# Performance work log

Hardware: AMD Instinct MI355X
Metric: run time of the kernel (lower is better)

## Reference

```python
import jax, jax.numpy as jnp
import numpy as np

N, DIM_V, DIM_MM, DIM_O = 1024, 2048, 64, 2048
EPS_LOG = 1e-3


def setup_inputs() -> dict:
    key = jax.random.key(0)
    ks = jax.random.split(key, 12)
    feature_visual = jax.random.normal(ks[0], (N, DIM_V), dtype=jnp.float32)
    # valid boxes (x1, y1, x2, y2) inside an ~800x600 image
    x1 = jax.random.uniform(ks[1], (N, 1)) * 700.0
    y1 = jax.random.uniform(ks[2], (N, 1)) * 500.0
    w = jax.random.uniform(ks[3], (N, 1)) * 180.0 + 16.0
    h = jax.random.uniform(ks[4], (N, 1)) * 180.0 + 16.0
    rois = jnp.concatenate([x1, y1, x1 + w, y1 + h], axis=1)
    s = 0.02
    return {
        "feature_visual": feature_visual,
        "rois": rois,
        "Wk": jax.random.normal(ks[5], (DIM_V, DIM_MM), dtype=jnp.float32) * s,
        "bk": jnp.zeros((DIM_MM,), jnp.float32),
        "Wq": jax.random.normal(ks[6], (DIM_V, DIM_MM), dtype=jnp.float32) * s,
        "bq": jnp.zeros((DIM_MM,), jnp.float32),
        "Wv": jax.random.normal(ks[7], (DIM_V, DIM_O), dtype=jnp.float32) * s,
        "bv": jnp.zeros((DIM_O,), jnp.float32),
        "G1": jax.random.normal(ks[8], (4, DIM_MM), dtype=jnp.float32) * s,
        "g1": jnp.zeros((DIM_MM,), jnp.float32),
        "G2": jax.random.normal(ks[9], (DIM_MM, 1), dtype=jnp.float32) * s,
        "g2": jnp.zeros((1,), jnp.float32),
    }


def _geometry_weight(rois, G1, g1, G2, g2):
    # pairwise relative geometry features [N, N, 4], then MLP -> ReLU scalar weight [N, N]
    wh = rois[:, 2:4] - rois[:, 0:2]                      # [N, 2] box width/height
    ctr = 0.5 * (rois[:, 0:2] + rois[:, 2:4])             # [N, 2] centers
    d = ctr[None, :, :] - ctr[:, None, :]                 # [N, N, 2] (j relative to i)
    f12 = jnp.log(jnp.abs(d) / wh[:, None, :] + EPS_LOG)  # log(|dx|/wi), log(|dy|/hi)
    f34 = jnp.log(wh[None, :, :] / wh[:, None, :])        # log(wj/wi), log(hj/hi)
    geo = jnp.concatenate([f12, f34], axis=-1)            # [N, N, 4]
    h = jax.nn.relu(jnp.einsum('ijf,fm->ijm', geo, G1) + g1)
    w = jax.nn.relu(jnp.einsum('ijm,mo->ijo', h, G2) + g2)
    return w[..., 0]                                      # [N, N]


def reference(feature_visual, rois, Wk, bk, Wq, bq, Wv, bv, G1, g1, G2, g2):
    fv = jax.nn.relu(feature_visual)                      # pre-activation features
    k = fv @ Wk + bk                                      # [N, dim_mm]
    q = fv @ Wq + bq                                      # [N, dim_mm]
    v = fv @ Wv + bv                                      # [N, dim_o]
    scale = 1.0 / np.sqrt(DIM_MM).astype(np.float32)
    visual_weight = (q @ k.T) * scale                     # [N, N]: score[i,j] = <q_i... wait
    # torch: (query.unsqueeze(0) * key.unsqueeze(1)).sum(2) -> score[i,j] = <k_i, q_j>
    visual_weight = (k @ q.T) * scale
    geometry_weight = _geometry_weight(rois, G1, g1, G2, g2)
    attention = jnp.exp(visual_weight) * geometry_weight  # [N, N]
    n = attention.shape[0]
    attention = attention * (1.0 - jnp.eye(n, dtype=attention.dtype))  # zero diagonal
    attention = attention / (attention.sum(axis=1, keepdims=True) + 1e-10)
    return attention @ v                                  # [N, dim_o]
```

## Files before the change

kernel.cpp:

```cpp
#include <hip/hip_runtime.h>
#include <hip/hip_bf16.h>

#define NR 1024
#define DV 2048
#define DMM 64
#define DO 2048

typedef __attribute__((ext_vector_type(8))) __bf16 bf16x8;
typedef __attribute__((ext_vector_type(4))) float f32x4;

__device__ __forceinline__ float relu_f(float x) { return fmaxf(x, 0.f); }

__device__ __forceinline__ unsigned short f2bf(float x) {
    union { float f; unsigned int u; } v; v.f = x;
    unsigned int r = v.u + 0x7fffu + ((v.u >> 16) & 1u);
    return (unsigned short)(r >> 16);
}

__device__ __forceinline__ void gload_lds16(const void* g, void* l) {
    __builtin_amdgcn_global_load_lds(
        (const __attribute__((address_space(1))) void*)g,
        (__attribute__((address_space(3))) void*)l, 16, 0, 0);
}

__device__ __forceinline__ void transpose_tile(
    const float* __restrict__ W, unsigned short* __restrict__ Wt,
    int Ncols, int k0, int o0, float (*ld)[65])
{
    const int t = threadIdx.x;
    const int r = t >> 2;
    const int c0 = (t & 3) * 16;
    #pragma unroll
    for (int i = 0; i < 4; ++i) {
        float4 v = *reinterpret_cast<const float4*>(&W[(size_t)(k0 + r) * Ncols + o0 + c0 + i * 4]);
        ld[c0 + i * 4 + 0][r] = v.x;
        ld[c0 + i * 4 + 1][r] = v.y;
        ld[c0 + i * 4 + 2][r] = v.z;
        ld[c0 + i * 4 + 3][r] = v.w;
    }
    __syncthreads();
    const int o = t >> 2;
    const int kc = (t & 3) * 16;
    unsigned int u[8];
    #pragma unroll
    for (int j = 0; j < 8; ++j) {
        float x0 = ld[o][kc + 2 * j], x1 = ld[o][kc + 2 * j + 1];
        u[j] = (unsigned)f2bf(x0) | ((unsigned)f2bf(x1) << 16);
    }
    uint4* dst = reinterpret_cast<uint4*>(&Wt[(size_t)(o0 + o) * DV + k0 + kc]);
    dst[0] = make_uint4(u[0], u[1], u[2], u[3]);
    dst[1] = make_uint4(u[4], u[5], u[6], u[7]);
}

__global__ __launch_bounds__(256) void prep_kernel(
    const float* __restrict__ feat,
    const float* __restrict__ Wk, const float* __restrict__ Wq, const float* __restrict__ Wv,
    const float* __restrict__ rois,
    unsigned short* __restrict__ fvb, unsigned short* __restrict__ WkqT,
    unsigned short* __restrict__ WvT,
    float4* __restrict__ boxf, float2* __restrict__ boxinv)
{
    __shared__ float ld[64][65];
    const int bid = blockIdx.x;
    if (bid < 1024) {
        const int idx = bid * 256 + threadIdx.x;
        const float4 a = *reinterpret_cast<const float4*>(feat + (size_t)idx * 8);
        const float4 b = *reinterpret_cast<const float4*>(feat + (size_t)idx * 8 + 4);
        uint4 o;
        o.x = (unsigned)f2bf(relu_f(a.x)) | ((unsigned)f2bf(relu_f(a.y)) << 16);
        o.y = (unsigned)f2bf(relu_f(a.z)) | ((unsigned)f2bf(relu_f(a.w)) << 16);
        o.z = (unsigned)f2bf(relu_f(b.x)) | ((unsigned)f2bf(relu_f(b.y)) << 16);
        o.w = (unsigned)f2bf(relu_f(b.z)) | ((unsigned)f2bf(relu_f(b.w)) << 16);
        *reinterpret_cast<uint4*>(fvb + (size_t)idx * 8) = o;
    } else if (bid < 2048) {
        const int idx = bid - 1024;
        transpose_tile(Wv, WvT, DO, (idx >> 5) * 64, (idx & 31) * 64, ld);
    } else if (bid < 2080) {
        transpose_tile(Wk, WkqT, DMM, (bid - 2048) * 64, 0, ld);
    } else if (bid < 2112) {
        transpose_tile(Wq, WkqT + 64 * DV, DMM, (bid - 2080) * 64, 0, ld);
    } else {
        const int idx = (bid - 2112) * 256 + threadIdx.x;
        const float4 r = *reinterpret_cast<const float4*>(rois + (size_t)idx * 4);
        const float w = r.z - r.x, h = r.w - r.y;
        boxf[idx]   = make_float4(0.5f * (r.x + r.z), 0.5f * (r.y + r.w), __logf(w), __logf(h));
        boxinv[idx] = make_float2(1.f / w, 1.f / h);
    }
}

template<int NT, int LDA, int LDB, int BNR>
__device__ __forceinline__ void mfma_tile_pipe(
    const unsigned short* __restrict__ A, const unsigned short* __restrict__ Bt,
    int bm0, int bn0, unsigned short* As, unsigned short* Bs, f32x4 (&acc)[2][BNR])
{
    const int t = threadIdx.x;
    const int w = t >> 6, lane = t & 63;
    const int wr = w >> 1, wc = w & 1;
    const int fr = lane & 15, fq = lane >> 4;
    const int sr = lane >> 3;
    const int sc = ((lane & 7) ^ sr) * 8;

    const unsigned short* ga0 = A + (size_t)(bm0 + w * 16 + 0 + sr) * LDA + sc;
    const unsigned short* ga1 = A + (size_t)(bm0 + w * 16 + 8 + sr) * LDA + sc;
    const unsigned short* gb[BNR];
    #pragma unroll
    for (int g = 0; g < BNR; ++g)
        gb[g] = Bt + (size_t)(bn0 + w * (BNR * 8) + g * 8 + sr) * LDB + sc;

#define STAGE(buf, ts_) do {                                                   \
        const size_t ko_ = (size_t)(ts_) * 64;                                 \
        gload_lds16(ga0 + ko_, &As[(buf) * 4096 + w * 1024]);                  \
        gload_lds16(ga1 + ko_, &As[(buf) * 4096 + w * 1024 + 512]);            \
        _Pragma("unroll")                                                      \
        for (int g = 0; g < BNR; ++g)                                          \
            gload_lds16(gb[g] + ko_,                                           \
                &Bs[(buf) * (BNR * 2048) + w * (BNR * 512) + g * 512]);        \
    } while (0)

#define COMPUTE(buf) do {                                                                     \
        const int kx_ = fr & 7;                                                               \
        const int clo_ = (fq ^ kx_) * 8, chi_ = ((fq + 4) ^ kx_) * 8;                         \
        bf16x8 afl[2], afh[2], bfl[BNR], bfh[BNR];                                            \
        _Pragma("unroll")                                                                     \
        for (int m = 0; m < 2; ++m) {                                                         \
            const int rb = (buf) * 4096 + (wr * 32 + m * 16 + fr) * 64;                       \
            afl[m] = *reinterpret_cast<const bf16x8*>(&As[rb + clo_]);                        \
            afh[m] = *reinterpret_cast<const bf16x8*>(&As[rb + chi_]);                        \
        }                                                                                     \
        _Pragma("unroll")                                                                     \
        for (int n = 0; n < BNR; ++n) {                                                       \
            const int cb = (buf) * (BNR * 2048) + (wc * (BNR * 16) + n * 16 + fr) * 64;       \
            bfl[n] = *reinterpret_cast<const bf16x8*>(&Bs[cb + clo_]);                        \
            bfh[n] = *reinterpret_cast<const bf16x8*>(&Bs[cb + chi_]);                        \
        }                                                                                     \
        _Pragma("unroll")                                                                     \
        for (int m = 0; m < 2; ++m)                                                           \
            _Pragma("unroll")                                                                 \
            for (int n = 0; n < BNR; ++n) {                                                   \
                acc[m][n] = __builtin_amdgcn_mfma_f32_16x16x32_bf16(afl[m], bfl[n], acc[m][n], 0, 0, 0); \
                acc[m][n] = __builtin_amdgcn_mfma_f32_16x16x32_bf16(afh[m], bfh[n], acc[m][n], 0, 0, 0); \
            }                                                                                 \
    } while (0)

    STAGE(0, 0);
    if (NT > 1) STAGE(1, 1);

    #pragma unroll 2
    for (int ts = 0; ts < NT - 1; ++ts) {
        if (BNR == 4) { asm volatile("s_waitcnt vmcnt(6)" ::: "memory"); }
        else          { asm volatile("s_waitcnt vmcnt(4)" ::: "memory"); }
        asm volatile("s_barrier" ::: "memory");
        COMPUTE(ts & 1);
        asm volatile("s_barrier" ::: "memory");
        if (ts + 2 < NT) STAGE(ts & 1, ts + 2);
    }
    asm volatile("s_waitcnt vmcnt(0)" ::: "memory");
    asm volatile("s_barrier" ::: "memory");
    COMPUTE((NT - 1) & 1);
#undef STAGE
#undef COMPUTE
}

__global__ __launch_bounds__(256) void gemm_vt_kq(
    const unsigned short* __restrict__ WvT, const unsigned short* __restrict__ fvb,
    const unsigned short* __restrict__ WkqT,
    const float* __restrict__ bv, const float* __restrict__ bk, const float* __restrict__ bq,
    unsigned short* __restrict__ vT, unsigned short* __restrict__ kqb)
{
    __shared__ unsigned short As[2 * 64 * 64];
    __shared__ unsigned short Bs[2 * 64 * 64];
    const int bid = blockIdx.x;
    const bool is_kq = bid >= 512;
    const unsigned short* A  = is_kq ? fvb  : WvT;
    const unsigned short* Bt = is_kq ? WkqT : fvb;
    const int bm0 = is_kq ? ((bid - 512) >> 1) * 64 : (bid >> 4) * 64;
    const int bn0 = is_kq ? ((bid - 512) & 1) * 64 : (bid & 15) * 64;

    f32x4 acc[2][2] = {};
    mfma_tile_pipe<DV / 64, DV, DV, 2>(A, Bt, bm0, bn0, As, Bs, acc);

    const int t = threadIdx.x;
    const int w = t >> 6, lane = t & 63;
    const int wr = w >> 1, wc = w & 1;
    const int fr = lane & 15, fq = lane >> 4;
    if (!is_kq) {
        #pragma unroll
        for (int m = 0; m < 2; ++m)
            #pragma unroll
            for (int r = 0; r < 4; ++r) {
                const int row = bm0 + wr * 32 + m * 16 + fq * 4 + r;
                const float badd = bv[row];
                #pragma unroll
                for (int n = 0; n < 2; ++n) {
                    const int col = bn0 + wc * 32 + n * 16 + fr;
                    vT[(size_t)row * NR + col] = f2bf(acc[m][n][r] + badd);
                }
            }
    } else {
        #pragma unroll
        for (int m = 0; m < 2; ++m)
            #pragma unroll
            for (int r = 0; r < 4; ++r) {
                const int row = bm0 + wr * 32 + m * 16 + fq * 4 + r;
                #pragma unroll
                for (int n = 0; n < 2; ++n) {
                    const int col = bn0 + wc * 32 + n * 16 + fr;
                    const float badd = (col < 64) ? bk[col] : bq[col - 64];
                    kqb[(size_t)row * 128 + col] = f2bf(acc[m][n][r] + badd);
                }
            }
    }
}

__global__ __launch_bounds__(256) void gemm_s(
    const unsigned short* __restrict__ kqb, float* __restrict__ S)
{
    __shared__ unsigned short As[64 * 64];
    __shared__ unsigned short Bs[128 * 64];
    const int bm0 = blockIdx.y * 64;
    const int bn0 = blockIdx.x * 128;
    f32x4 acc[2][4] = {};
    mfma_tile_pipe<1, 128, 128, 4>(kqb, kqb + 64, bm0, bn0, As, Bs, acc);
    const int t = threadIdx.x;
    const int w = t >> 6, lane = t & 63;
    const int wr = w >> 1, wc = w & 1;
    const int fr = lane & 15, fq = lane >> 4;
    #pragma unroll
    for (int m = 0; m < 2; ++m)
        #pragma unroll
        for (int r = 0; r < 4; ++r) {
            const int row = bm0 + wr * 32 + m * 16 + fq * 4 + r;
            #pragma unroll
            for (int n = 0; n < 4; ++n) {
                const int col = bn0 + wc * 64 + n * 16 + fr;
                S[(size_t)row * NR + col] = acc[m][n][r] * 0.125f;
            }
        }
}

__global__ __launch_bounds__(256) void gemm_out(
    const unsigned short* __restrict__ attb, const unsigned short* __restrict__ vT,
    float* __restrict__ out)
{
    __shared__ unsigned short As[2 * 64 * 64];
    __shared__ unsigned short Bs[2 * 64 * 64];
    const int bid = blockIdx.x;
    const int bm0 = (bid >> 5) * 64;
    const int bn0 = (bid & 31) * 64;
    f32x4 acc[2][2] = {};
    mfma_tile_pipe<NR / 64, NR, NR, 2>(attb, vT, bm0, bn0, As, Bs, acc);
    const int t = threadIdx.x;
    const int w = t >> 6, lane = t & 63;
    const int wr = w >> 1, wc = w & 1;
    const int fr = lane & 15, fq = lane >> 4;
    #pragma unroll
    for (int m = 0; m < 2; ++m)
        #pragma unroll
        for (int r = 0; r < 4; ++r) {
            const int row = bm0 + wr * 32 + m * 16 + fq * 4 + r;
            #pragma unroll
            for (int n = 0; n < 2; ++n) {
                const int col = bn0 + wc * 32 + n * 16 + fr;
                out[(size_t)row * DO + col] = acc[m][n][r];
            }
        }
}

#define MLP_STEP(A_, B_, C_, D_, E_, F_)                                            \
    {                                                                               \
        float h_ = fmaf(ff1[ch], A_, fmaf(ff2[ch], B_, fmaf(ff3[ch], C_,            \
                   fmaf(ff4[ch], D_, E_))));                                        \
        h_ = fmaxf(h_, 0.f);                                                        \
        gw[ch] = fmaf(h_, F_, gw[ch]);                                              \
    }

__global__ __launch_bounds__(256) void attn_kernel(
    const float* __restrict__ S,
    const float4* __restrict__ boxf, const float2* __restrict__ boxinv,
    const float* __restrict__ G1, const float* __restrict__ g1,
    const float* __restrict__ G2, const float* __restrict__ g2,
    unsigned short* __restrict__ att)
{
    __shared__ float G1s[4][64];
    __shared__ float g1s[64];
    __shared__ float G2s[64];
    __shared__ float red[4];
    const int i = blockIdx.x;
    const int t = threadIdx.x;
    if (t < 64) {
        G1s[0][t] = G1[t];
        G1s[1][t] = G1[64 + t];
        G1s[2][t] = G1[128 + t];
        G1s[3][t] = G1[192 + t];
        g1s[t] = g1[t];
        G2s[t] = G2[t];
    }
    __syncthreads();
    const float4 bi = boxf[i];
    const float2 ivi = boxinv[i];
    const float g2v = g2[0];

    float ff1[4], ff2[4], ff3[4], ff4[4], sc[4], gw[4] = {0.f, 0.f, 0.f, 0.f};
    #pragma unroll
    for (int ch = 0; ch < 4; ++ch) {
        const int j = ch * 256 + t;
        const float4 bj = boxf[j];
        sc[ch] = S[(size_t)i * NR + j];
        ff1[ch] = __logf(fmaf(fabsf(bj.x - bi.x), ivi.x, 1e-3f));
        ff2[ch] = __logf(fmaf(fabsf(bj.y - bi.y), ivi.y, 1e-3f));
        ff3[ch] = bj.z - bi.z;
        ff4[ch] = bj.w - bi.w;
    }

    for (int mt = 0; mt < 64; mt += 8) {
        const float4 A0 = *reinterpret_cast<const float4*>(&G1s[0][mt]);
        const float4 A1 = *reinterpret_cast<const float4*>(&G1s[0][mt + 4]);
        const float4 B0 = *reinterpret_cast<const float4*>(&G1s[1][mt]);
        const float4 B1 = *reinterpret_cast<const float4*>(&G1s[1][mt + 4]);
        const float4 C0 = *reinterpret_cast<const float4*>(&G1s[2][mt]);
        const float4 C1 = *reinterpret_cast<const float4*>(&G1s[2][mt + 4]);
        const float4 D0 = *reinterpret_cast<const float4*>(&G1s[3][mt]);
        const float4 D1 = *reinterpret_cast<const float4*>(&G1s[3][mt + 4]);
        const float4 E0 = *reinterpret_cast<const float4*>(&g1s[mt]);
        const float4 E1 = *reinterpret_cast<const float4*>(&g1s[mt + 4]);
        const float4 F0 = *reinterpret_cast<const float4*>(&G2s[mt]);
        const float4 F1 = *reinterpret_cast<const float4*>(&G2s[mt + 4]);
        #pragma unroll
        for (int ch = 0; ch < 4; ++ch) {
            MLP_STEP(A0.x, B0.x, C0.x, D0.x, E0.x, F0.x)
            MLP_STEP(A0.y, B0.y, C0.y, D0.y, E0.y, F0.y)
            MLP_STEP(A0.z, B0.z, C0.z, D0.z, E0.z, F0.z)
            MLP_STEP(A0.w, B0.w, C0.w, D0.w, E0.w, F0.w)
            MLP_STEP(A1.x, B1.x, C1.x, D1.x, E1.x, F1.x)
            MLP_STEP(A1.y, B1.y, C1.y, D1.y, E1.y, F1.y)
            MLP_STEP(A1.z, B1.z, C1.z, D1.z, E1.z, F1.z)
            MLP_STEP(A1.w, B1.w, C1.w, D1.w, E1.w, F1.w)
        }
    }

    float vals[4];
    float rsum = 0.f;
    #pragma unroll
    for (int ch = 0; ch < 4; ++ch) {
        const float gwp = fmaxf(gw[ch] + g2v, 0.f);
        float a = __expf(sc[ch]) * gwp;
        if (ch * 256 + t == i) a = 0.f;
        vals[ch] = a;
        rsum += a;
    }
    #pragma unroll
    for (int o = 32; o > 0; o >>= 1) rsum += __shfl_down(rsum, o, 64);
    if ((t & 63) == 0) red[t >> 6] = rsum;
    __syncthreads();
    const float inv = 1.f / (red[0] + red[1] + red[2] + red[3] + 1e-10f);
    #pragma unroll
    for (int ch = 0; ch < 4; ++ch)
        att[(size_t)i * NR + ch * 256 + t] = f2bf(vals[ch] * inv);
}

extern "C" void kernel_launch(void* const* d_in, const int* in_sizes, int n_in,
                              void* d_out, int out_size, void* d_ws, size_t ws_size,
                              hipStream_t stream) {
    const float* feat = (const float*)d_in[0];
    const float* rois = (const float*)d_in[1];
    const float* Wk   = (const float*)d_in[2];
    const float* bk   = (const float*)d_in[3];
    const float* Wq   = (const float*)d_in[4];
    const float* bq   = (const float*)d_in[5];
    const float* Wv   = (const float*)d_in[6];
    const float* bv   = (const float*)d_in[7];
    const float* G1   = (const float*)d_in[8];
    const float* g1   = (const float*)d_in[9];
    const float* G2   = (const float*)d_in[10];
    const float* g2   = (const float*)d_in[11];
    float* out = (float*)d_out;
    char* ws = (char*)d_ws;

    unsigned short* kqb  = (unsigned short*)ws;
    float4* boxf         = (float4*)(ws + (256 << 10));
    float2* boxinv       = (float2*)(ws + (272 << 10));
    unsigned short* fvb  = (unsigned short*)(ws + (512 << 10));
    unsigned short* WvT  = (unsigned short*)(ws + (512 << 10) + (4 << 20));
    unsigned short* WkqT = (unsigned short*)(ws + (512 << 10) + (12 << 20));
    unsigned short* vT   = (unsigned short*)(ws + (1024 << 10) + (12 << 20));
    unsigned short* attb = (unsigned short*)(ws + (1024 << 10) + (16 << 20));
    float* Sbuf          = (float*)(ws + (1024 << 10) + (18 << 20));

    prep_kernel<<<2116, 256, 0, stream>>>(feat, Wk, Wq, Wv, rois, fvb, WkqT, WvT, boxf, boxinv);
    gemm_vt_kq<<<544, 256, 0, stream>>>(WvT, fvb, WkqT, bv, bk, bq, vT, kqb);
    gemm_s<<<dim3(8, 16), 256, 0, stream>>>(kqb, Sbuf);
    attn_kernel<<<NR, 256, 0, stream>>>(Sbuf, boxf, boxinv, G1, g1, G2, g2, attb);
    gemm_out<<<512, 256, 0, stream>>>(attb, vT, out);
}
```

Measured before the change: 57.66 us.

## Move geometry MLP into prep kernel, fuse exp-mask into score GEMM, defer normalization

After: 63.94 us. 10.9% more time.

```diff
diff --git a/kernel.cpp b/kernel.cpp
--- a/kernel.cpp
+++ b/kernel.cpp
@@ -22,6 +22,14 @@
         (const __attribute__((address_space(1))) void*)g,
         (__attribute__((address_space(3))) void*)l, 16, 0, 0);
 }
+
+#define MLP_STEP(A_, B_, C_, D_, E_, F_)                                            \
+    {                                                                               \
+        float h_ = fmaf(ff1[ch], A_, fmaf(ff2[ch], B_, fmaf(ff3[ch], C_,            \
+                   fmaf(ff4[ch], D_, E_))));                                        \
+        h_ = fmaxf(h_, 0.f);                                                        \
+        gw[ch] = fmaf(h_, F_, gw[ch]);                                              \
+    }
 
 __device__ __forceinline__ void transpose_tile(
     const float* __restrict__ W, unsigned short* __restrict__ Wt,
@@ -56,14 +64,19 @@
     const float* __restrict__ feat,
     const float* __restrict__ Wk, const float* __restrict__ Wq, const float* __restrict__ Wv,
     const float* __restrict__ rois,
+    const float* __restrict__ G1, const float* __restrict__ g1,
+    const float* __restrict__ G2, const float* __restrict__ g2,
     unsigned short* __restrict__ fvb, unsigned short* __restrict__ WkqT,
-    unsigned short* __restrict__ WvT,
-    float4* __restrict__ boxf, float2* __restrict__ boxinv)
+    unsigned short* __restrict__ WvT, float* __restrict__ g)
 {
     __shared__ float ld[64][65];
+    __shared__ float G1s[4][64];
+    __shared__ float g1s[64];
+    __shared__ float G2s[64];
     const int bid = blockIdx.x;
+    const int t = threadIdx.x;
     if (bid < 1024) {
-        const int idx = bid * 256 + threadIdx.x;
+        const int idx = bid * 256 + t;
         const float4 a = *reinterpret_cast<const float4*>(feat + (size_t)idx * 8);
         const float4 b = *reinterpret_cast<const float4*>(feat + (size_t)idx * 8 + 4);
         uint4 o;
@@ -80,11 +93,61 @@
     } else if (bid < 2112) {
         transpose_tile(Wq, WkqT + 64 * DV, DMM, (bid - 2080) * 64, 0, ld);
     } else {
-        const int idx = (bid - 2112) * 256 + threadIdx.x;
-        const float4 r = *reinterpret_cast<const float4*>(rois + (size_t)idx * 4);
-        const float w = r.z - r.x, h = r.w - r.y;
-        boxf[idx]   = make_float4(0.5f * (r.x + r.z), 0.5f * (r.y + r.w), __logf(w), __logf(h));
-        boxinv[idx] = make_float2(1.f / w, 1.f / h);
+        const int i = bid - 2112;
+        if (t < 64) {
+            G1s[0][t] = G1[t];
+            G1s[1][t] = G1[64 + t];
+            G1s[2][t] = G1[128 + t];
+            G1s[3][t] = G1[192 + t];
+            g1s[t] = g1[t];
+            G2s[t] = G2[t];
+        }
+        __syncthreads();
+        const float4 ri = *reinterpret_cast<const float4*>(rois + (size_t)i * 4);
+        const float wi = ri.z - ri.x, hi_ = ri.w - ri.y;
+        const float cxi = 0.5f * (ri.x + ri.z), cyi = 0.5f * (ri.y + ri.w);
+        const float iwi = 1.f / wi, ihi = 1.f / hi_;
+        const float g2v = g2[0];
+
+        float ff1[4], ff2[4], ff3[4], ff4[4], gw[4] = {0.f, 0.f, 0.f, 0.f};
+        #pragma unroll
+        for (int ch = 0; ch < 4; ++ch) {
+            const int j = ch * 256 + t;
+            const float4 rj = *reinterpret_cast<const float4*>(rois + (size_t)j * 4);
+            const float wj = rj.z - rj.x, hj = rj.w - rj.y;
+            ff1[ch] = __logf(fmaf(fabsf(0.5f * (rj.x + rj.z) - cxi), iwi, 1e-3f));
+            ff2[ch] = __logf(fmaf(fabsf(0.5f * (rj.y + rj.w) - cyi), ihi, 1e-3f));
+            ff3[ch] = __logf(wj * iwi);
+            ff4[ch] = __logf(hj * ihi);
+        }
+        for (int mt = 0; mt < 64; mt += 8) {
+            const float4 A0 = *reinterpret_cast<const float4*>(&G1s[0][mt]);
+            const float4 A1 = *reinterpret_cast<const float4*>(&G1s[0][mt + 4]);
+            const float4 B0 = *reinterpret_cast<const float4*>(&G1s[1][mt]);
+            const float4 B1 = *reinterpret_cast<const float4*>(&G1s[1][mt + 4]);
+            const float4 C0 = *reinterpret_cast<const float4*>(&G1s[2][mt]);
+            const float4 C1 = *reinterpret_cast<const float4*>(&G1s[2][mt + 4]);
+            const float4 D0 = *reinterpret_cast<const float4*>(&G1s[3][mt]);
+            const float4 D1 = *reinterpret_cast<const float4*>(&G1s[3][mt + 4]);
+            const float4 E0 = *reinterpret_cast<const float4*>(&g1s[mt]);
+            const float4 E1 = *reinterpret_cast<const float4*>(&g1s[mt + 4]);
+            const float4 F0 = *reinterpret_cast<const float4*>(&G2s[mt]);
+            const float4 F1 = *reinterpret_cast<const float4*>(&G2s[mt + 4]);
+            #pragma unroll
+            for (int ch = 0; ch < 4; ++ch) {
+                MLP_STEP(A0.x, B0.x, C0.x, D0.x, E0.x, F0.x)
+                MLP_STEP(A0.y, B0.y, C0.y, D0.y, E0.y, F0.y)
+                MLP_STEP(A0.z, B0.z, C0.z, D0.z, E0.z, F0.z)
+                MLP_STEP(A0.w, B0.w, C0.w, D0.w, E0.w, F0.w)
+                MLP_STEP(A1.x, B1.x, C1.x, D1.x, E1.x, F1.x)
+                MLP_STEP(A1.y, B1.y, C1.y, D1.y, E1.y, F1.y)
+                MLP_STEP(A1.z, B1.z, C1.z, D1.z, E1.z, F1.z)
+                MLP_STEP(A1.w, B1.w, C1.w, D1.w, E1.w, F1.w)
+            }
+        }
+        #pragma unroll
+        for (int ch = 0; ch < 4; ++ch)
+            g[(size_t)i * NR + ch * 256 + t] = fmaxf(gw[ch] + g2v, 0.f);
     }
 }
 
@@ -212,44 +275,98 @@
     }
 }
 
-__global__ __launch_bounds__(256) void gemm_s(
-    const unsigned short* __restrict__ kqb, float* __restrict__ S)
+__global__ __launch_bounds__(256) void s_att(
+    const unsigned short* __restrict__ kqb, const float* __restrict__ g,
+    unsigned short* __restrict__ att, float* __restrict__ partial)
 {
     __shared__ unsigned short As[64 * 64];
-    __shared__ unsigned short Bs[128 * 64];
-    const int bm0 = blockIdx.y * 64;
-    const int bn0 = blockIdx.x * 128;
-    f32x4 acc[2][4] = {};
-    mfma_tile_pipe<1, 128, 128, 4>(kqb, kqb + 64, bm0, bn0, As, Bs, acc);
+    __shared__ unsigned short Bs[64 * 64];
+    __shared__ float srow[2][64];
     const int t = threadIdx.x;
     const int w = t >> 6, lane = t & 63;
     const int wr = w >> 1, wc = w & 1;
     const int fr = lane & 15, fq = lane >> 4;
+    const int sr = lane >> 3;
+    const int sc = ((lane & 7) ^ sr) * 8;
+    const int bm0 = blockIdx.y * 64;
+    const int bn0 = blockIdx.x * 64;
+
+    gload_lds16(kqb + (size_t)(bm0 + w * 16 + 0 + sr) * 128 + sc, &As[w * 1024]);
+    gload_lds16(kqb + (size_t)(bm0 + w * 16 + 8 + sr) * 128 + sc, &As[w * 1024 + 512]);
+    gload_lds16(kqb + 64 + (size_t)(bn0 + w * 16 + 0 + sr) * 128 + sc, &Bs[w * 1024]);
+    gload_lds16(kqb + 64 + (size_t)(bn0 + w * 16 + 8 + sr) * 128 + sc, &Bs[w * 1024 + 512]);
+    asm volatile("s_waitcnt vmcnt(0)" ::: "memory");
+    asm volatile("s_barrier" ::: "memory");
+
+    const int kx = fr & 7;
+    const int clo = (fq ^ kx) * 8, chi = ((fq + 4) ^ kx) * 8;
+    f32x4 acc[2][2] = {};
+    bf16x8 afl[2], afh[2], bfl[2], bfh[2];
+    #pragma unroll
+    for (int m = 0; m < 2; ++m) {
+        const int rb = (wr * 32 + m * 16 + fr) * 64;
+        afl[m] = *reinterpret_cast<const bf16x8*>(&As[rb + clo]);
+        afh[m] = *reinterpret_cast<const bf16x8*>(&As[rb + chi]);
+    }
+    #pragma unroll
+    for (int n = 0; n < 2; ++n) {
+        const int cb = (wc * 32 + n * 16 + fr) * 64;
+        bfl[n] = *reinterpret_cast<const bf16x8*>(&Bs[cb + clo]);
+        bfh[n] = *reinterpret_cast<const bf16x8*>(&Bs[cb + chi]);
+    }
+    #pragma unroll
+    for (int m = 0; m < 2; ++m)
+        #pragma unroll
+        for (int n = 0; n < 2; ++n) {
+            acc[m][n] = __builtin_amdgcn_mfma_f32_16x16x32_bf16(afl[m], bfl[n], acc[m][n], 0, 0, 0);
+            acc[m][n] = __builtin_amdgcn_mfma_f32_16x16x32_bf16(afh[m], bfh[n], acc[m][n], 0, 0, 0);
+        }
+
     #pragma unroll
     for (int m = 0; m < 2; ++m)
         #pragma unroll
         for (int r = 0; r < 4; ++r) {
             const int row = bm0 + wr * 32 + m * 16 + fq * 4 + r;
-            #pragma unroll
-            for (int n = 0; n < 4; ++n) {
-                const int col = bn0 + wc * 64 + n * 16 + fr;
-                S[(size_t)row * NR + col] = acc[m][n][r] * 0.125f;
+            float rs = 0.f;
+            #pragma unroll
+            for (int n = 0; n < 2; ++n) {
+                const int col = bn0 + wc * 32 + n * 16 + fr;
+                float a = __expf(acc[m][n][r] * 0.125f) * g[(size_t)row * NR + col];
+                if (row == col) a = 0.f;
+                att[(size_t)row * NR + col] = f2bf(a);
+                rs += a;
             }
-        }
+            #pragma unroll
+            for (int o = 1; o < 16; o <<= 1) rs += __shfl_xor(rs, o, 64);
+            if (fr == 0) srow[wc][wr * 32 + m * 16 + fq * 4 + r] = rs;
+        }
+    __syncthreads();
+    if (t < 64)
+        partial[(size_t)blockIdx.x * NR + bm0 + t] = srow[0][t] + srow[1][t];
 }
 
 __global__ __launch_bounds__(256) void gemm_out(
     const unsigned short* __restrict__ attb, const unsigned short* __restrict__ vT,
-    float* __restrict__ out)
+    const float* __restrict__ partial, float* __restrict__ out)
 {
     __shared__ unsigned short As[2 * 64 * 64];
     __shared__ unsigned short Bs[2 * 64 * 64];
+    __shared__ float sinv[64];
     const int bid = blockIdx.x;
     const int bm0 = (bid >> 5) * 64;
     const int bn0 = (bid & 31) * 64;
     f32x4 acc[2][2] = {};
     mfma_tile_pipe<NR / 64, NR, NR, 2>(attb, vT, bm0, bn0, As, Bs, acc);
-    const int t = threadIdx.x;
+
+    const int t = threadIdx.x;
+    if (t < 64) {
+        float s = 0.f;
+        #pragma unroll
+        for (int c = 0; c < 16; ++c) s += partial[(size_t)c * NR + bm0 + t];
+        sinv[t] = 1.f / (s + 1e-10f);
+    }
+    __syncthreads();
+
     const int w = t >> 6, lane = t & 63;
     const int wr = w >> 1, wc = w & 1;
     const int fr = lane & 15, fq = lane >> 4;
@@ -257,105 +374,15 @@
     for (int m = 0; m < 2; ++m)
         #pragma unroll
         for (int r = 0; r < 4; ++r) {
-            const int row = bm0 + wr * 32 + m * 16 + fq * 4 + r;
+            const int rl = wr * 32 + m * 16 + fq * 4 + r;
+            const int row = bm0 + rl;
+            const float sc_ = sinv[rl];
             #pragma unroll
             for (int n = 0; n < 2; ++n) {
                 const int col = bn0 + wc * 32 + n * 16 + fr;
-                out[(size_t)row * DO + col] = acc[m][n][r];
+                out[(size_t)row * DO + col] = acc[m][n][r] * sc_;
             }
         }
-}
-
-#define MLP_STEP(A_, B_, C_, D_, E_, F_)                                            \
-    {                                                                               \
-        float h_ = fmaf(ff1[ch], A_, fmaf(ff2[ch], B_, fmaf(ff3[ch], C_,            \
-                   fmaf(ff4[ch], D_, E_))));                                        \
-        h_ = fmaxf(h_, 0.f);                                                        \
-        gw[ch] = fmaf(h_, F_, gw[ch]);                                              \
-    }
-
-__global__ __launch_bounds__(256) void attn_kernel(
-    const float* __restrict__ S,
-    const float4* __restrict__ boxf, const float2* __restrict__ boxinv,
-    const float* __restrict__ G1, const float* __restrict__ g1,
-    const float* __restrict__ G2, const float* __restrict__ g2,
-    unsigned short* __restrict__ att)
-{
-    __shared__ float G1s[4][64];
-    __shared__ float g1s[64];
-    __shared__ float G2s[64];
-    __shared__ float red[4];
-    const int i = blockIdx.x;
-    const int t = threadIdx.x;
-    if (t < 64) {
-        G1s[0][t] = G1[t];
-        G1s[1][t] = G1[64 + t];
-        G1s[2][t] = G1[128 + t];
-        G1s[3][t] = G1[192 + t];
-        g1s[t] = g1[t];
-        G2s[t] = G2[t];
-    }
-    __syncthreads();
-    const float4 bi = boxf[i];
-    const float2 ivi = boxinv[i];
-    const float g2v = g2[0];
-
-    float ff1[4], ff2[4], ff3[4], ff4[4], sc[4], gw[4] = {0.f, 0.f, 0.f, 0.f};
-    #pragma unroll
-    for (int ch = 0; ch < 4; ++ch) {
-        const int j = ch * 256 + t;
-        const float4 bj = boxf[j];
-        sc[ch] = S[(size_t)i * NR + j];
-        ff1[ch] = __logf(fmaf(fabsf(bj.x - bi.x), ivi.x, 1e-3f));
-        ff2[ch] = __logf(fmaf(fabsf(bj.y - bi.y), ivi.y, 1e-3f));
-        ff3[ch] = bj.z - bi.z;
-        ff4[ch] = bj.w - bi.w;
-    }
-
-    for (int mt = 0; mt < 64; mt += 8) {
-        const float4 A0 = *reinterpret_cast<const float4*>(&G1s[0][mt]);
-        const float4 A1 = *reinterpret_cast<const float4*>(&G1s[0][mt + 4]);
-        const float4 B0 = *reinterpret_cast<const float4*>(&G1s[1][mt]);
-        const float4 B1 = *reinterpret_cast<const float4*>(&G1s[1][mt + 4]);
-        const float4 C0 = *reinterpret_cast<const float4*>(&G1s[2][mt]);
-        const float4 C1 = *reinterpret_cast<const float4*>(&G1s[2][mt + 4]);
-        const float4 D0 = *reinterpret_cast<const float4*>(&G1s[3][mt]);
-        const float4 D1 = *reinterpret_cast<const float4*>(&G1s[3][mt + 4]);
-        const float4 E0 = *reinterpret_cast<const float4*>(&g1s[mt]);
-        const float4 E1 = *reinterpret_cast<const float4*>(&g1s[mt + 4]);
-        const float4 F0 = *reinterpret_cast<const float4*>(&G2s[mt]);
-        const float4 F1 = *reinterpret_cast<const float4*>(&G2s[mt + 4]);
-        #pragma unroll
-        for (int ch = 0; ch < 4; ++ch) {
-            MLP_STEP(A0.x, B0.x, C0.x, D0.x, E0.x, F0.x)
-            MLP_STEP(A0.y, B0.y, C0.y, D0.y, E0.y, F0.y)
-            MLP_STEP(A0.z, B0.z, C0.z, D0.z, E0.z, F0.z)
-            MLP_STEP(A0.w, B0.w, C0.w, D0.w, E0.w, F0.w)
-            MLP_STEP(A1.x, B1.x, C1.x, D1.x, E1.x, F1.x)
-            MLP_STEP(A1.y, B1.y, C1.y, D1.y, E1.y, F1.y)
-            MLP_STEP(A1.z, B1.z, C1.z, D1.z, E1.z, F1.z)
-            MLP_STEP(A1.w, B1.w, C1.w, D1.w, E1.w, F1.w)
-        }
-    }
-
-    float vals[4];
-    float rsum = 0.f;
-    #pragma unroll
-    for (int ch = 0; ch < 4; ++ch) {
-        const float gwp = fmaxf(gw[ch] + g2v, 0.f);
-        float a = __expf(sc[ch]) * gwp;
-        if (ch * 256 + t == i) a = 0.f;
-        vals[ch] = a;
-        rsum += a;
-    }
-    #pragma unroll
-    for (int o = 32; o > 0; o >>= 1) rsum += __shfl_down(rsum, o, 64);
-    if ((t & 63) == 0) red[t >> 6] = rsum;
-    __syncthreads();
-    const float inv = 1.f / (red[0] + red[1] + red[2] + red[3] + 1e-10f);
-    #pragma unroll
-    for (int ch = 0; ch < 4; ++ch)
-        att[(size_t)i * NR + ch * 256 + t] = f2bf(vals[ch] * inv);
 }
 
 extern "C" void kernel_launch(void* const* d_in, const int* in_sizes, int n_in,
@@ -377,18 +404,17 @@
     char* ws = (char*)d_ws;
 
     unsigned short* kqb  = (unsigned short*)ws;
-    float4* boxf         = (float4*)(ws + (256 << 10));
-    float2* boxinv       = (float2*)(ws + (272 << 10));
-    unsigned short* fvb  = (unsigned short*)(ws + (512 << 10));
-    unsigned short* WvT  = (unsigned short*)(ws + (512 << 10) + (4 << 20));
-    unsigned short* WkqT = (unsigned short*)(ws + (512 << 10) + (12 << 20));
-    unsigned short* vT   = (unsigned short*)(ws + (1024 << 10) + (12 << 20));
-    unsigned short* attb = (unsigned short*)(ws + (1024 << 10) + (16 << 20));
-    float* Sbuf          = (float*)(ws + (1024 << 10) + (18 << 20));
-
-    prep_kernel<<<2116, 256, 0, stream>>>(feat, Wk, Wq, Wv, rois, fvb, WkqT, WvT, boxf, boxinv);
+    float* partial       = (float*)(ws + (256 << 10));
+    float* gbuf          = (float*)(ws + (1 << 20));
+    unsigned short* fvb  = (unsigned short*)(ws + (5 << 20));
+    unsigned short* WvT  = (unsigned short*)(ws + (9 << 20));
+    unsigned short* WkqT = (unsigned short*)(ws + (17 << 20));
+    unsigned short* vT   = (unsigned short*)(ws + (18 << 20));
+    unsigned short* attb = (unsigned short*)(ws + (22 << 20));
+
+    prep_kernel<<<3136, 256, 0, stream>>>(feat, Wk, Wq, Wv, rois, G1, g1, G2, g2,
+                                          fvb, WkqT, WvT, gbuf);
     gemm_vt_kq<<<544, 256, 0, stream>>>(WvT, fvb, WkqT, bv, bk, bq, vT, kqb);
-    gemm_s<<<dim3(8, 16), 256, 0, stream>>>(kqb, Sbuf);
-    attn_kernel<<<NR, 256, 0, stream>>>(Sbuf, boxf, boxinv, G1, g1, G2, g2, attb);
-    gemm_out<<<512, 256, 0, stream>>>(attb, vT, out);
-}
+    s_att<<<dim3(16, 16), 256, 0, stream>>>(kqb, gbuf, attb, partial);
+    gemm_out<<<512, 256, 0, stream>>>(attb, vT, partial, out);
+}
```
